# Kernel tuning notes

Measured on AMD Instinct MI355X. Metric: run time of the kernel, lower is better.

## Reference

```python
import jax, jax.numpy as jnp
import numpy as np

NUM_C = 100
DIM_S = 128
SIZE_M = 64
EMB = 128
MAX_CODE_LEN = 128
NODE_COUNT = 10000
PATH_COUNT = 10000
B, L = 16, 128


def setup_inputs() -> dict:
    key = jax.random.key(0)
    ks = jax.random.split(key, 24)
    def nrm(k, shape, fan):
        return jax.random.normal(k, shape, jnp.float32) * np.float32(np.sqrt(2.0 / fan))
    code = jax.random.randint(ks[0], (B, L, NUM_C * 2 + MAX_CODE_LEN * 3), 0, 10000)
    q = jax.random.randint(ks[1], (B, L), 0, NUM_C)
    r = jax.random.randint(ks[2], (B, L), 0, 2 * NUM_C)
    return {
        "code": code, "q": q, "r": r,
        "embed_nodes": nrm(ks[3], (NODE_COUNT + 2, EMB), EMB),
        "embed_paths": nrm(ks[4], (PATH_COUNT + 2, EMB), EMB),
        "W_pt": nrm(ks[5], (3 * EMB, 3 * EMB), 3 * EMB), "b_pt": jnp.zeros((3 * EMB,), jnp.float32),
        "W_att": nrm(ks[6], (3 * EMB, 1), 3 * EMB), "b_att": jnp.zeros((1,), jnp.float32),
        "k_emb": nrm(ks[7], (NUM_C + 1, DIM_S), DIM_S),
        "Mk": nrm(ks[8], (SIZE_M, DIM_S), DIM_S),
        "Mv0": nrm(ks[9], (SIZE_M, DIM_S), DIM_S),
        "v_emb": nrm(ks[10], (NUM_C * 2 + 2, DIM_S), DIM_S),
        "W_e": nrm(ks[11], (4 * DIM_S, DIM_S), 4 * DIM_S), "b_e": jnp.zeros((DIM_S,), jnp.float32),
        "W_a": nrm(ks[12], (4 * DIM_S, DIM_S), 4 * DIM_S), "b_a": jnp.zeros((DIM_S,), jnp.float32),
        "W_f": nrm(ks[13], (2 * DIM_S, DIM_S), 2 * DIM_S), "b_f": jnp.zeros((DIM_S,), jnp.float32),
        "W_p": nrm(ks[14], (DIM_S, 10), DIM_S), "b_p": jnp.zeros((10,), jnp.float32),
    }


def reference(code, q, r, embed_nodes, embed_paths, W_pt, b_pt, W_att, b_att,
              k_emb, Mk, Mv0, v_emb, W_e, b_e, W_a, b_a, W_f, b_f, W_p, b_p):
    bsz = code.shape[0]
    k = k_emb[q]                                    # [B,L,D]
    vr = v_emb[r]                                   # [B,L,D]
    # code2vec path triples: [B,L,MAX_CODE_LEN,3] = (start, path, end)
    c2v = code[:, :, NUM_C * 2:].reshape(bsz, code.shape[1], MAX_CODE_LEN, 3)
    full = jnp.concatenate([embed_nodes[c2v[..., 0]],
                            embed_nodes[c2v[..., 2]],
                            embed_paths[c2v[..., 1]]], axis=3)   # [B,L,P,3E]
    tr = jnp.tanh(full @ W_pt + b_pt)
    cw = tr @ W_att + b_att                          # [B,L,P,1]
    attn = jax.nn.softmax(cw, axis=1)                # faithful: softmax over seq dim (dim=1)
    code_vec = jnp.sum(full * attn, axis=2)          # [B,L,3E]
    v = jnp.concatenate([vr, code_vec], axis=2)      # [B,L,4D]
    w = jax.nn.softmax(k @ Mk.T, axis=-1)            # [B,L,M]
    e = jax.nn.sigmoid(v @ W_e + b_e)                # [B,L,D]
    a = jnp.tanh(v @ W_a + b_a)                      # [B,L,D]
    Mvt0 = jnp.broadcast_to(Mv0, (bsz,) + Mv0.shape) # [B,M,D]

    def step(Mvt, inp):
        et, at, wt = inp                             # [B,D],[B,D],[B,M]
        read = jnp.einsum('bm,bmd->bd', wt, Mvt)     # read pre-update memory (Mv[:, :-1])
        Mvt = Mvt * (1.0 - wt[:, :, None] * et[:, None, :]) + wt[:, :, None] * at[:, None, :]
        return Mvt, read

    _, reads = jax.lax.scan(step, Mvt0,
                            (e.transpose(1, 0, 2), a.transpose(1, 0, 2), w.transpose(1, 0, 2)))
    read = reads.transpose(1, 0, 2)                  # [B,L,D]
    f = jnp.tanh(jnp.concatenate([read, k], axis=-1) @ W_f + b_f)
    # dropout is identity in eval mode
    return jax.nn.sigmoid(f @ W_p + b_p)             # [B,L,10]
```

## Files before the change

### kernel.cpp

```cpp
#include <hip/hip_runtime.h>


typedef unsigned char u8;
typedef unsigned short u16;
typedef unsigned int u32;
typedef __attribute__((ext_vector_type(8))) short short8;
typedef __attribute__((ext_vector_type(4))) float f32x4;
typedef __attribute__((ext_vector_type(2))) float f32x2;

#define DEV __device__ __forceinline__
#define LOG2E 1.4426950408889634f

DEV u16 f2b(float f) {
    union { float f; u32 i; } v; v.f = f;
    u32 x = v.i;
    u32 r = (x + 0x7FFFu + ((x >> 16) & 1u)) >> 16;
    return (u16)r;
}
DEV float nexp(float x) { return __builtin_amdgcn_exp2f(x * LOG2E); }
DEV float nrcp(float x) { return __builtin_amdgcn_rcpf(x); }
DEV float fast_tanh(float x) {
    return 1.f - 2.f * nrcp(1.f + __builtin_amdgcn_exp2f(x * (2.f * LOG2E)));
}
DEV float sigmoidf_(float x) { return nrcp(1.f + __builtin_amdgcn_exp2f(-x * LOG2E)); }
DEV f32x2 d8(u32 x, bool hi) {
    return hi ? __builtin_amdgcn_cvt_pk_f32_fp8((int)x, true)
              : __builtin_amdgcn_cvt_pk_f32_fp8((int)x, false);
}
DEV u8 e8(float x) {
    return (u8)(__builtin_amdgcn_cvt_pk_fp8_f32(x, x, 0, false) & 0xFF);
}

__global__ void k_conv(const float* __restrict__ EN, const float* __restrict__ EP,
                       const float* __restrict__ Wpt, const float* __restrict__ We,
                       const float* __restrict__ Wa, const float* __restrict__ Wf,
                       const float* __restrict__ Wp,
                       u16* __restrict__ ENb, u16* __restrict__ EPb, u16* __restrict__ Wt,
                       u16* __restrict__ WeaT, u16* __restrict__ WfT, u16* __restrict__ WpT,
                       u8* __restrict__ EN8, u8* __restrict__ EP8) {
    const int NE = 10002 * 128;
    const int T0 = 2 * NE;
    const int T1 = T0 + 147456;
    const int T2 = T1 + 131072;
    const int T3 = T2 + 32768;
    const int T4 = T3 + 2048;
    const int T5 = T4 + NE / 2;
    const int T6 = T5 + NE / 2;
    for (int i = blockIdx.x * blockDim.x + threadIdx.x; i < T6; i += gridDim.x * blockDim.x) {
        if (i < NE) {
            ENb[i] = f2b(EN[i]);
        } else if (i < T0) {
            EPb[i - NE] = f2b(EP[i - NE]);
        } else if (i < T1) {
            int w = i - T0;  u32 n = (u32)w / 384u, k = (u32)w % 384u;
            Wt[w] = f2b(Wpt[k * 384 + n]);
        } else if (i < T2) {
            int w = i - T1;  int n = w >> 9, k = w & 511;
            WeaT[w] = f2b((n < 128) ? We[k * 128 + n] : Wa[k * 128 + (n - 128)]);
        } else if (i < T3) {
            int w = i - T2;  int n = w >> 8, k = w & 255;
            WfT[w] = f2b(Wf[k * 128 + n]);
        } else if (i < T4) {
            int w = i - T3;  int n = w >> 7, k = w & 127;
            WpT[w] = (n < 10) ? f2b(Wp[k * 10 + n]) : (u16)0;
        } else if (i < T5) {
            int j = i - T4;
            int pk = __builtin_amdgcn_cvt_pk_fp8_f32(EN[2 * j], EN[2 * j + 1], 0, false);
            ((u16*)EN8)[j] = (u16)pk;
        } else {
            int j = i - T5;
            int pk = __builtin_amdgcn_cvt_pk_fp8_f32(EP[2 * j], EP[2 * j + 1], 0, false);
            ((u16*)EP8)[j] = (u16)pk;
        }
    }
}

__global__ void k_wsm(const float* __restrict__ Kemb, const float* __restrict__ Mk,
                      float* __restrict__ wsmall) {
    int row = blockIdx.x;
    int m = threadIdx.x;
    __shared__ float kr[128];
    kr[m] = Kemb[row * 128 + m];
    kr[64 + m] = Kemb[row * 128 + 64 + m];
    __syncthreads();
    float lg = 0.f;
    for (int k = 0; k < 128; k += 8) {
        float mk8[8];
#pragma unroll
        for (int u = 0; u < 8; u++) mk8[u] = Mk[m * 128 + k + u];
#pragma unroll
        for (int u = 0; u < 8; u++) lg = fmaf(kr[k + u], mk8[u], lg);
    }
    float mx = lg;
#pragma unroll
    for (int off = 32; off; off >>= 1) mx = fmaxf(mx, __shfl_xor(mx, off, 64));
    float ex = nexp(lg - mx);
    float sum = ex;
#pragma unroll
    for (int off = 32; off; off >>= 1) sum += __shfl_xor(sum, off, 64);
    wsmall[row * 64 + m] = ex * nrcp(sum);
}

__global__ void k_preM(const u16* __restrict__ ENb, const u16* __restrict__ EPb,
                       const u16* __restrict__ Wt, const float* __restrict__ bpt,
                       u8* __restrict__ PS8, u8* __restrict__ PE8, u8* __restrict__ PP8) {
    int which = blockIdx.y;
    int r0 = blockIdx.x * 16;
    int wv = threadIdx.x >> 6, lane = threadIdx.x & 63;
    int m = lane & 15, quad = lane >> 4;
    const u16* A = (which == 2) ? EPb : ENb;
    int koff = which * 128;
    u8* dst = (which == 0) ? PS8 : (which == 1) ? PE8 : PP8;

    const short8* ap = (const short8*)(A + (r0 + m) * 128 + quad * 8);
    short8 a0 = ap[0], a1 = ap[4], a2 = ap[8], a3 = ap[12];

    for (int nt = 0; nt < 6; nt++) {
        int n0 = wv * 96 + nt * 16;
        const short8* bp = (const short8*)(Wt + (n0 + m) * 384 + koff + quad * 8);
        f32x4 acc = {0.f, 0.f, 0.f, 0.f};
        acc = __builtin_amdgcn_mfma_f32_16x16x32_bf16(a0, bp[0],  acc, 0, 0, 0);
        acc = __builtin_amdgcn_mfma_f32_16x16x32_bf16(a1, bp[4],  acc, 0, 0, 0);
        acc = __builtin_amdgcn_mfma_f32_16x16x32_bf16(a2, bp[8],  acc, 0, 0, 0);
        acc = __builtin_amdgcn_mfma_f32_16x16x32_bf16(a3, bp[12], acc, 0, 0, 0);
        int col = n0 + m;
        float bias = (which == 2) ? bpt[col] : 0.f;
#pragma unroll
        for (int reg = 0; reg < 4; reg++) {
            int row = r0 + quad * 4 + reg;
            if (row < 10002) dst[row * 384 + col] = e8(acc[reg] + bias);
        }
    }
}

__global__ void k_cw(const int* __restrict__ code,
                     const u8* __restrict__ PS8, const u8* __restrict__ PE8,
                     const u8* __restrict__ PP8, const float* __restrict__ Watt,
                     const float* __restrict__ batt, float* __restrict__ cw) {
    int wv = threadIdx.x >> 6, lane = threadIdx.x & 63;
    int t0 = (blockIdx.x * 4 + wv) * 4;
    int b = t0 >> 14;
    int rem = t0 & 16383;
    int l = rem >> 7, p0 = rem & 127;

    const int* c = code + ((b * 128 + l) * 584 + 200 + 3 * p0);
    int si[4], pi[4], ei[4];
#pragma unroll
    for (int i = 0; i < 4; i++) {
        si[i] = __builtin_amdgcn_readfirstlane(c[3 * i]);
        pi[i] = __builtin_amdgcn_readfirstlane(c[3 * i + 1]);
        ei[i] = __builtin_amdgcn_readfirstlane(c[3 * i + 2]);
    }

    int j0 = 6 * lane;
    int o32 = j0 + ((lane & 1) << 1);
    int o16 = j0 + ((~lane & 1) << 2);
    float wa0 = Watt[o32], wa1 = Watt[o32 + 1], wa2 = Watt[o32 + 2], wa3 = Watt[o32 + 3];
    float wb0 = Watt[o16], wb1 = Watt[o16 + 1];
    float batt0 = batt[0];

#pragma unroll
    for (int i = 0; i < 4; i++) {
        const u8* bs = PS8 + si[i] * 384;
        const u8* be = PE8 + ei[i] * 384;
        const u8* bq = PP8 + pi[i] * 384;
        u32 xs = *(const u32*)(bs + o32), ys = *(const u16*)(bs + o16);
        u32 xe = *(const u32*)(be + o32), ye = *(const u16*)(be + o16);
        u32 xq = *(const u32*)(bq + o32), yq = *(const u16*)(bq + o16);

        f32x2 zA = d8(xs, false) + d8(xe, false) + d8(xq, false);
        f32x2 zB = d8(xs, true)  + d8(xe, true)  + d8(xq, true);
        f32x2 zC = d8(ys, false) + d8(ye, false) + d8(yq, false);

        float acc = 0.f;
        acc = fmaf(fast_tanh(zA.x), wa0, acc);
        acc = fmaf(fast_tanh(zA.y), wa1, acc);
        acc = fmaf(fast_tanh(zB.x), wa2, acc);
        acc = fmaf(fast_tanh(zB.y), wa3, acc);
        acc = fmaf(fast_tanh(zC.x), wb0, acc);
        acc = fmaf(fast_tanh(zC.y), wb1, acc);

#pragma unroll
        for (int off = 32; off; off >>= 1) acc += __shfl_down(acc, off, 64);
        if (lane == 0) cw[(b * 128 + p0 + i) * 128 + l] = acc + batt0;
    }
}

__global__ void k_sm(const float* __restrict__ cw, float* __restrict__ attn) {
    int b = blockIdx.x >> 3, p0 = (blockIdx.x & 7) * 16;
    int tid = threadIdx.x;
    int wv = tid >> 6, lane = tid & 63;
    __shared__ float tile[16][128];
    __shared__ float atile[128][17];
    for (int idx = tid; idx < 2048; idx += 256) {
        int pp = idx >> 7, l = idx & 127;
        tile[pp][l] = cw[(b * 128 + p0 + pp) * 128 + l];
    }
    __syncthreads();
#pragma unroll
    for (int pl = 0; pl < 4; pl++) {
        int pp = wv * 4 + pl;
        float x0 = tile[pp][lane], x1 = tile[pp][64 + lane];
        float mx = fmaxf(x0, x1);
#pragma unroll
        for (int off = 32; off; off >>= 1) mx = fmaxf(mx, __shfl_xor(mx, off, 64));
        float e0 = nexp(x0 - mx), e1 = nexp(x1 - mx);
        float sum = e0 + e1;
#pragma unroll
        for (int off = 32; off; off >>= 1) sum += __shfl_xor(sum, off, 64);
        float inv = nrcp(sum);
        atile[lane][pp] = e0 * inv;
        atile[64 + lane][pp] = e1 * inv;
    }
    __syncthreads();
    for (int idx = tid; idx < 2048; idx += 256) {
        int l = idx >> 4, pp = idx & 15;
        attn[(b * 128 + l) * 128 + p0 + pp] = atile[l][pp];
    }
}

__global__ void k_cv(const int* __restrict__ code, const float* __restrict__ attn,
                     const u8* __restrict__ EN8, const u8* __restrict__ EP8,
                     const int* __restrict__ rr, const int* __restrict__ qq,
                     const float* __restrict__ Vemb, const float* __restrict__ Kemb,
                     u16* __restrict__ vA, u16* __restrict__ fA) {
    int row = blockIdx.x;
    int tid = threadIdx.x;
    int wv = tid >> 6, lane = tid & 63;
    __shared__ int si[128], ei[128], pi[128];
    __shared__ float at[128];
    __shared__ float part[4][3][128];
    if (tid < 128) {
        const int* c = code + (row * 584 + 200);
        si[tid] = c[3 * tid]; pi[tid] = c[3 * tid + 1]; ei[tid] = c[3 * tid + 2];
        at[tid] = attn[row * 128 + tid];
    }
    if (tid < 128) {
        vA[row * 512 + tid] = f2b(Vemb[rr[row] * 128 + tid]);
    } else {
        int t2 = tid - 128;
        fA[row * 256 + 128 + t2] = f2b(Kemb[qq[row] * 128 + t2]);
    }
    __syncthreads();
    float a0 = 0.f, a1 = 0.f, b0 = 0.f, b1 = 0.f, c0 = 0.f, c1 = 0.f;
    int o = 2 * lane;
    for (int p = wv; p < 128; p += 8) {
        int p2 = p + 4;
        float w = at[p], w2 = at[p2];
        u32 us = *(const u16*)(EN8 + si[p] * 128 + o);
        u32 ue = *(const u16*)(EN8 + ei[p] * 128 + o);
        u32 up = *(const u16*)(EP8 + pi[p] * 128 + o);
        u32 vs = *(const u16*)(EN8 + si[p2] * 128 + o);
        u32 ve = *(const u16*)(EN8 + ei[p2] * 128 + o);
        u32 vp = *(const u16*)(EP8 + pi[p2] * 128 + o);
        f32x2 fs = d8(us, false), fe = d8(ue, false), fp = d8(up, false);
        f32x2 gs = d8(vs, false), ge = d8(ve, false), gp = d8(vp, false);
        a0 = fmaf(w, fs.x, a0); a1 = fmaf(w, fs.y, a1);
        b0 = fmaf(w, fe.x, b0); b1 = fmaf(w, fe.y, b1);
        c0 = fmaf(w, fp.x, c0); c1 = fmaf(w, fp.y, c1);
        a0 = fmaf(w2, gs.x, a0); a1 = fmaf(w2, gs.y, a1);
        b0 = fmaf(w2, ge.x, b0); b1 = fmaf(w2, ge.y, b1);
        c0 = fmaf(w2, gp.x, c0); c1 = fmaf(w2, gp.y, c1);
    }
    part[wv][0][2 * lane] = a0; part[wv][0][2 * lane + 1] = a1;
    part[wv][1][2 * lane] = b0; part[wv][1][2 * lane + 1] = b1;
    part[wv][2][2 * lane] = c0; part[wv][2][2 * lane + 1] = c1;
    __syncthreads();
    u16* vrow = vA + row * 512 + 128;
    for (int idx = tid; idx < 384; idx += 256) {
        int tbl = idx >> 7, col = idx & 127;
        vrow[idx] = f2b(part[0][tbl][col] + part[1][tbl][col] + part[2][tbl][col] + part[3][tbl][col]);
    }
}

__global__ void k_eawM(const u16* __restrict__ vA, const u16* __restrict__ WeaT,
                       const float* __restrict__ be, const float* __restrict__ ba,
                       float* __restrict__ eb, float* __restrict__ ab) {
    int rt = blockIdx.x >> 2, cg = blockIdx.x & 3;
    int wv = threadIdx.x >> 6, lane = threadIdx.x & 63;
    int ct = cg * 4 + wv;
    int m = lane & 15, quad = lane >> 4;
    const short8* ap = (const short8*)(vA + (rt * 16 + m) * 512 + quad * 8);
    const short8* bp = (const short8*)(WeaT + (ct * 16 + m) * 512 + quad * 8);
    f32x4 acc = {0.f, 0.f, 0.f, 0.f};
#pragma unroll
    for (int kc = 0; kc < 16; kc++)
        acc = __builtin_amdgcn_mfma_f32_16x16x32_bf16(ap[kc * 4], bp[kc * 4], acc, 0, 0, 0);
    int col = ct * 16 + m;
    bool isA = col >= 128;
    int c2 = isA ? col - 128 : col;
    float bias = isA ? ba[c2] : be[c2];
#pragma unroll
    for (int reg = 0; reg < 4; reg++) {
        int row = rt * 16 + quad * 4 + reg;
        float val = acc[reg] + bias;
        if (isA) ab[row * 128 + c2] = fast_tanh(val);
        else     eb[row * 128 + c2] = sigmoidf_(val);
    }
}

__global__ void k_scan(const float* __restrict__ Mv0, const float* __restrict__ eb,
                       const float* __restrict__ ab, const float* __restrict__ wsmall,
                       const int* __restrict__ qq, u16* __restrict__ fA) {
    int b = blockIdx.x >> 4, dblk = blockIdx.x & 15;
    int lane = threadIdx.x;
    int s = lane >> 3, dlo = lane & 7;
    int d = dblk * 8 + dlo;

    __shared__ float wsm[101 * 64];
    __shared__ float el[128][8];
    __shared__ float al[128][8];
    __shared__ int ql[128];

    for (int i = lane; i < 101 * 64; i += 64) wsm[i] = wsmall[i];
    for (int i = lane; i < 1024; i += 64) {
        int t = i >> 3, dl = i & 7;
        el[t][dl] = eb[(b * 128 + t) * 128 + dblk * 8 + dl];
        al[t][dl] = ab[(b * 128 + t) * 128 + dblk * 8 + dl];
    }
    for (int i = lane; i < 128; i += 64) ql[i] = qq[b * 128 + i];
    __syncthreads();

    float mv[8];
#pragma unroll
    for (int q = 0; q < 8; q++) mv[q] = Mv0[(s * 8 + q) * 128 + d];

    u16* fout = fA + (b * 128) * 256 + d;

    int qt = ql[0];
    const float4* wr = (const float4*)(wsm + qt * 64 + s * 8);
    float4 w0 = wr[0], w1 = wr[1];
    float ecur = el[0][dlo], acur = al[0][dlo];

    for (int t = 0; t < 128; t++) {
        int tn = (t < 127) ? t + 1 : 127;
        int qn = ql[tn];
        const float4* wrn = (const float4*)(wsm + qn * 64 + s * 8);
        float4 nw0 = wrn[0], nw1 = wrn[1];
        float en = el[tn][dlo], an = al[tn][dlo];

        float w[8] = { w0.x, w0.y, w0.z, w0.w, w1.x, w1.y, w1.z, w1.w };
        float rd = 0.f;
#pragma unroll
        for (int q = 0; q < 8; q++) {
            rd = fmaf(w[q], mv[q], rd);
            mv[q] = fmaf(w[q], fmaf(-mv[q], ecur, acur), mv[q]);
        }
        rd += __shfl_xor(rd, 8, 64);
        rd += __shfl_xor(rd, 16, 64);
        rd += __shfl_xor(rd, 32, 64);
        if (s == 0) fout[t * 256] = f2b(rd);

        ecur = en; acur = an; w0 = nw0; w1 = nw1;
    }
}

__global__ void k_outM(const u16* __restrict__ fA, const u16* __restrict__ WfT,
                       const float* __restrict__ bfp, u16* __restrict__ gA) {
    int rt = blockIdx.x >> 1, cg = blockIdx.x & 1;
    int wv = threadIdx.x >> 6, lane = threadIdx.x & 63;
    int ct = cg * 4 + wv;
    int m = lane & 15, quad = lane >> 4;
    const short8* ap = (const short8*)(fA + (rt * 16 + m) * 256 + quad * 8);
    const short8* bp = (const short8*)(WfT + (ct * 16 + m) * 256 + quad * 8);
    f32x4 acc = {0.f, 0.f, 0.f, 0.f};
#pragma unroll
    for (int kc = 0; kc < 8; kc++)
        acc = __builtin_amdgcn_mfma_f32_16x16x32_bf16(ap[kc * 4], bp[kc * 4], acc, 0, 0, 0);
    int col = ct * 16 + m;
    float bias = bfp[col];
#pragma unroll
    for (int reg = 0; reg < 4; reg++) {
        int row = rt * 16 + quad * 4 + reg;
        gA[row * 128 + col] = f2b(fast_tanh(acc[reg] + bias));
    }
}

__global__ void k_fin(const u16* __restrict__ gA, const u16* __restrict__ WpT,
                      const float* __restrict__ bp, float* __restrict__ out) {
    int wv = threadIdx.x >> 6, lane = threadIdx.x & 63;
    int rt = blockIdx.x * 4 + wv;
    int m = lane & 15, quad = lane >> 4;
    const short8* ap = (const short8*)(gA + (rt * 16 + m) * 128 + quad * 8);
    const short8* bp8 = (const short8*)(WpT + m * 128 + quad * 8);
    f32x4 acc = {0.f, 0.f, 0.f, 0.f};
#pragma unroll
    for (int kc = 0; kc < 4; kc++)
        acc = __builtin_amdgcn_mfma_f32_16x16x32_bf16(ap[kc * 4], bp8[kc * 4], acc, 0, 0, 0);
    if (m < 10) {
        float bias = bp[m];
#pragma unroll
        for (int reg = 0; reg < 4; reg++) {
            int row = rt * 16 + quad * 4 + reg;
            out[row * 10 + m] = sigmoidf_(acc[reg] + bias);
        }
    }
}

extern "C" void kernel_launch(void* const* d_in, const int* in_sizes, int n_in,
                              void* d_out, int out_size, void* d_ws, size_t ws_size,
                              hipStream_t stream) {
    const int*   code = (const int*)d_in[0];
    const int*   q    = (const int*)d_in[1];
    const int*   r    = (const int*)d_in[2];
    const float* EN   = (const float*)d_in[3];
    const float* EP   = (const float*)d_in[4];
    const float* Wpt  = (const float*)d_in[5];
    const float* bpt  = (const float*)d_in[6];
    const float* Watt = (const float*)d_in[7];
    const float* batt = (const float*)d_in[8];
    const float* Kemb = (const float*)d_in[9];
    const float* Mk   = (const float*)d_in[10];
    const float* Mv0  = (const float*)d_in[11];
    const float* Vemb = (const float*)d_in[12];
    const float* We   = (const float*)d_in[13];
    const float* be   = (const float*)d_in[14];
    const float* Wa   = (const float*)d_in[15];
    const float* ba   = (const float*)d_in[16];
    const float* Wf   = (const float*)d_in[17];
    const float* bf_  = (const float*)d_in[18];
    const float* Wp   = (const float*)d_in[19];
    const float* bp   = (const float*)d_in[20];

    char* ws = (char*)d_ws;
    size_t off = 0;
    auto alloc = [&](size_t bytes) { void* p = ws + off; off = (off + bytes + 255) & ~255UL; return p; };
    u8*    PS8    = (u8*)alloc(10002UL * 384);
    u8*    PE8    = (u8*)alloc(10002UL * 384);
    u8*    PP8    = (u8*)alloc(10002UL * 384);
    u16*   ENb    = (u16*)alloc(10002UL * 128 * 2);
    u16*   EPb    = (u16*)alloc(10016UL * 128 * 2);
    u8*    EN8    = (u8*)alloc(10002UL * 128);
    u8*    EP8    = (u8*)alloc(10002UL * 128);
    u16*   Wt     = (u16*)alloc(384UL * 384 * 2);
    u16*   WeaT   = (u16*)alloc(256UL * 512 * 2);
    u16*   WfT    = (u16*)alloc(128UL * 256 * 2);
    u16*   WpT    = (u16*)alloc(16UL * 128 * 2);
    float* cw     = (float*)alloc(16UL * 128 * 128 * 4);
    float* attn   = (float*)alloc(16UL * 128 * 128 * 4);
    u16*   vA     = (u16*)alloc(2048UL * 512 * 2);
    u16*   fA     = (u16*)alloc(2048UL * 256 * 2);
    u16*   gA     = (u16*)alloc(2048UL * 128 * 2);
    float* eb     = (float*)alloc(2048UL * 128 * 4);
    float* ab     = (float*)alloc(2048UL * 128 * 4);
    float* wsmall = (float*)alloc(101UL * 64 * 4);

    k_conv<<<2048, 256, 0, stream>>>(EN, EP, Wpt, We, Wa, Wf, Wp, ENb, EPb, Wt, WeaT, WfT, WpT, EN8, EP8);
    k_wsm<<<101, 64, 0, stream>>>(Kemb, Mk, wsmall);
    k_preM<<<dim3(626, 3), 256, 0, stream>>>(ENb, EPb, Wt, bpt, PS8, PE8, PP8);
    k_cw<<<16384, 256, 0, stream>>>(code, PS8, PE8, PP8, Watt, batt, cw);
    k_sm<<<128, 256, 0, stream>>>(cw, attn);
    k_cv<<<2048, 256, 0, stream>>>(code, attn, EN8, EP8, r, q, Vemb, Kemb, vA, fA);
    k_eawM<<<512, 256, 0, stream>>>(vA, WeaT, be, ba, eb, ab);
    k_scan<<<256, 64, 0, stream>>>(Mv0, eb, ab, wsmall, q, fA);
    k_outM<<<256, 256, 0, stream>>>(fA, WfT, bf_, gA);
    k_fin<<<32, 256, 0, stream>>>(gA, WpT, bp, (float*)d_out);
}
```

Baseline: 260.1 us.

## Fuse small kernels, batch cw gathers, fold tanh scale and drop constant softmax bias

Folds the k_wsm softmax into extra blocks of k_conv and merges the bf16 and fp8 embedding conversions into one pass over the fp32 tables. k_outM and k_fin become a single kernel that keeps the intermediate tile in shared memory. k_cw now handles 8 paths per wave with all gathers issued before compute, and folds the tanh 2*log2e scale into the fp8 precompute. It also drops the attention bias and rewrites tanh-dot as sigmoid weighted by -2*W, relying on softmax shift invariance. The aim is fewer launches, fewer global round trips and more memory-level parallelism, at the cost of more registers in k_cw and a small fp8 precision shift from the pre-scaling.

```diff
diff --git a/kernel.cpp b/kernel.cpp
--- a/kernel.cpp
+++ b/kernel.cpp
@@ -10,6 +10,7 @@
 
 #define DEV __device__ __forceinline__
 #define LOG2E 1.4426950408889634f
+#define KSCALE 2.8853900817779268f
 
 DEV u16 f2b(float f) {
     union { float f; u32 i; } v; v.f = f;
@@ -35,22 +36,50 @@
                        const float* __restrict__ Wpt, const float* __restrict__ We,
                        const float* __restrict__ Wa, const float* __restrict__ Wf,
                        const float* __restrict__ Wp,
-                       u16* __restrict__ ENb, u16* __restrict__ EPb, u16* __restrict__ Wt,
-                       u16* __restrict__ WeaT, u16* __restrict__ WfT, u16* __restrict__ WpT,
-                       u8* __restrict__ EN8, u8* __restrict__ EP8) {
-    const int NE = 10002 * 128;
-    const int T0 = 2 * NE;
+                       const float* __restrict__ Kemb, const float* __restrict__ Mk,
+                       u16* __restrict__ ENb, u16* __restrict__ EPb,
+                       u8* __restrict__ EN8, u8* __restrict__ EP8,
+                       u16* __restrict__ Wt, u16* __restrict__ WeaT,
+                       u16* __restrict__ WfT, u16* __restrict__ WpT,
+                       float* __restrict__ wsmall) {
+    if (blockIdx.x >= 2048) {
+        int wv = threadIdx.x >> 6, lane = threadIdx.x & 63;
+        int row = (blockIdx.x - 2048) * 4 + wv;
+        if (row >= 101) return;
+        float lg = 0.f;
+        for (int k = 0; k < 128; k += 8) {
+            float mk8[8];
+#pragma unroll
+            for (int u = 0; u < 8; u++) mk8[u] = Mk[lane * 128 + k + u];
+#pragma unroll
+            for (int u = 0; u < 8; u++) lg = fmaf(Kemb[row * 128 + k + u], mk8[u], lg);
+        }
+        float mx = lg;
+#pragma unroll
+        for (int off = 32; off; off >>= 1) mx = fmaxf(mx, __shfl_xor(mx, off, 64));
+        float ex = nexp(lg - mx);
+        float sum = ex;
+#pragma unroll
+        for (int off = 32; off; off >>= 1) sum += __shfl_xor(sum, off, 64);
+        wsmall[row * 64 + lane] = ex * nrcp(sum);
+        return;
+    }
+    const int NEH = 10002 * 64;
+    const int T0 = 2 * NEH;
     const int T1 = T0 + 147456;
     const int T2 = T1 + 131072;
     const int T3 = T2 + 32768;
     const int T4 = T3 + 2048;
-    const int T5 = T4 + NE / 2;
-    const int T6 = T5 + NE / 2;
-    for (int i = blockIdx.x * blockDim.x + threadIdx.x; i < T6; i += gridDim.x * blockDim.x) {
-        if (i < NE) {
-            ENb[i] = f2b(EN[i]);
+    for (int i = blockIdx.x * blockDim.x + threadIdx.x; i < T4; i += 2048 * blockDim.x) {
+        if (i < NEH) {
+            float a = EN[2 * i], b = EN[2 * i + 1];
+            ((u32*)ENb)[i] = ((u32)f2b(b) << 16) | f2b(a);
+            ((u16*)EN8)[i] = (u16)__builtin_amdgcn_cvt_pk_fp8_f32(a, b, 0, false);
         } else if (i < T0) {
-            EPb[i - NE] = f2b(EP[i - NE]);
+            int j = i - NEH;
+            float a = EP[2 * j], b = EP[2 * j + 1];
+            ((u32*)EPb)[j] = ((u32)f2b(b) << 16) | f2b(a);
+            ((u16*)EP8)[j] = (u16)__builtin_amdgcn_cvt_pk_fp8_f32(a, b, 0, false);
         } else if (i < T1) {
             int w = i - T0;  u32 n = (u32)w / 384u, k = (u32)w % 384u;
             Wt[w] = f2b(Wpt[k * 384 + n]);
@@ -60,45 +89,11 @@
         } else if (i < T3) {
             int w = i - T2;  int n = w >> 8, k = w & 255;
             WfT[w] = f2b(Wf[k * 128 + n]);
-        } else if (i < T4) {
+        } else {
             int w = i - T3;  int n = w >> 7, k = w & 127;
             WpT[w] = (n < 10) ? f2b(Wp[k * 10 + n]) : (u16)0;
-        } else if (i < T5) {
-            int j = i - T4;
-            int pk = __builtin_amdgcn_cvt_pk_fp8_f32(EN[2 * j], EN[2 * j + 1], 0, false);
-            ((u16*)EN8)[j] = (u16)pk;
-        } else {
-            int j = i - T5;
-            int pk = __builtin_amdgcn_cvt_pk_fp8_f32(EP[2 * j], EP[2 * j + 1], 0, false);
-            ((u16*)EP8)[j] = (u16)pk;
-        }
-    }
-}
-
-__global__ void k_wsm(const float* __restrict__ Kemb, const float* __restrict__ Mk,
-                      float* __restrict__ wsmall) {
-    int row = blockIdx.x;
-    int m = threadIdx.x;
-    __shared__ float kr[128];
-    kr[m] = Kemb[row * 128 + m];
-    kr[64 + m] = Kemb[row * 128 + 64 + m];
-    __syncthreads();
-    float lg = 0.f;
-    for (int k = 0; k < 128; k += 8) {
-        float mk8[8];
-#pragma unroll
-        for (int u = 0; u < 8; u++) mk8[u] = Mk[m * 128 + k + u];
-#pragma unroll
-        for (int u = 0; u < 8; u++) lg = fmaf(kr[k + u], mk8[u], lg);
-    }
-    float mx = lg;
-#pragma unroll
-    for (int off = 32; off; off >>= 1) mx = fmaxf(mx, __shfl_xor(mx, off, 64));
-    float ex = nexp(lg - mx);
-    float sum = ex;
-#pragma unroll
-    for (int off = 32; off; off >>= 1) sum += __shfl_xor(sum, off, 64);
-    wsmall[row * 64 + m] = ex * nrcp(sum);
+        }
+    }
 }
 
 __global__ void k_preM(const u16* __restrict__ ENb, const u16* __restrict__ EPb,
@@ -128,7 +123,7 @@
 #pragma unroll
         for (int reg = 0; reg < 4; reg++) {
             int row = r0 + quad * 4 + reg;
-            if (row < 10002) dst[row * 384 + col] = e8(acc[reg] + bias);
+            if (row < 10002) dst[row * 384 + col] = e8((acc[reg] + bias) * KSCALE);
         }
     }
 }
@@ -136,17 +131,17 @@
 __global__ void k_cw(const int* __restrict__ code,
                      const u8* __restrict__ PS8, const u8* __restrict__ PE8,
                      const u8* __restrict__ PP8, const float* __restrict__ Watt,
-                     const float* __restrict__ batt, float* __restrict__ cw) {
+                     float* __restrict__ cw) {
     int wv = threadIdx.x >> 6, lane = threadIdx.x & 63;
-    int t0 = (blockIdx.x * 4 + wv) * 4;
+    int t0 = (blockIdx.x * 4 + wv) * 8;
     int b = t0 >> 14;
     int rem = t0 & 16383;
     int l = rem >> 7, p0 = rem & 127;
 
     const int* c = code + ((b * 128 + l) * 584 + 200 + 3 * p0);
-    int si[4], pi[4], ei[4];
-#pragma unroll
-    for (int i = 0; i < 4; i++) {
+    int si[8], pi[8], ei[8];
+#pragma unroll
+    for (int i = 0; i < 8; i++) {
         si[i] = __builtin_amdgcn_readfirstlane(c[3 * i]);
         pi[i] = __builtin_amdgcn_readfirstlane(c[3 * i + 1]);
         ei[i] = __builtin_amdgcn_readfirstlane(c[3 * i + 2]);
@@ -155,34 +150,37 @@
     int j0 = 6 * lane;
     int o32 = j0 + ((lane & 1) << 1);
     int o16 = j0 + ((~lane & 1) << 2);
-    float wa0 = Watt[o32], wa1 = Watt[o32 + 1], wa2 = Watt[o32 + 2], wa3 = Watt[o32 + 3];
-    float wb0 = Watt[o16], wb1 = Watt[o16 + 1];
-    float batt0 = batt[0];
-
-#pragma unroll
-    for (int i = 0; i < 4; i++) {
+    float wa0 = -2.f * Watt[o32],     wa1 = -2.f * Watt[o32 + 1];
+    float wa2 = -2.f * Watt[o32 + 2], wa3 = -2.f * Watt[o32 + 3];
+    float wb0 = -2.f * Watt[o16],     wb1 = -2.f * Watt[o16 + 1];
+
+    u32 xs[8], ys[8], xe[8], ye[8], xq[8], yq[8];
+#pragma unroll
+    for (int i = 0; i < 8; i++) {
         const u8* bs = PS8 + si[i] * 384;
         const u8* be = PE8 + ei[i] * 384;
         const u8* bq = PP8 + pi[i] * 384;
-        u32 xs = *(const u32*)(bs + o32), ys = *(const u16*)(bs + o16);
-        u32 xe = *(const u32*)(be + o32), ye = *(const u16*)(be + o16);
-        u32 xq = *(const u32*)(bq + o32), yq = *(const u16*)(bq + o16);
-
-        f32x2 zA = d8(xs, false) + d8(xe, false) + d8(xq, false);
-        f32x2 zB = d8(xs, true)  + d8(xe, true)  + d8(xq, true);
-        f32x2 zC = d8(ys, false) + d8(ye, false) + d8(yq, false);
-
-        float acc = 0.f;
-        acc = fmaf(fast_tanh(zA.x), wa0, acc);
-        acc = fmaf(fast_tanh(zA.y), wa1, acc);
-        acc = fmaf(fast_tanh(zB.x), wa2, acc);
-        acc = fmaf(fast_tanh(zB.y), wa3, acc);
-        acc = fmaf(fast_tanh(zC.x), wb0, acc);
-        acc = fmaf(fast_tanh(zC.y), wb1, acc);
+        xs[i] = *(const u32*)(bs + o32); ys[i] = *(const u16*)(bs + o16);
+        xe[i] = *(const u32*)(be + o32); ye[i] = *(const u16*)(be + o16);
+        xq[i] = *(const u32*)(bq + o32); yq[i] = *(const u16*)(bq + o16);
+    }
+
+#pragma unroll
+    for (int i = 0; i < 8; i++) {
+        f32x2 zA = d8(xs[i], false) + d8(xe[i], false) + d8(xq[i], false);
+        f32x2 zB = d8(xs[i], true)  + d8(xe[i], true)  + d8(xq[i], true);
+        f32x2 zC = d8(ys[i], false) + d8(ye[i], false) + d8(yq[i], false);
+
+        float acc = nrcp(1.f + __builtin_amdgcn_exp2f(zA.x)) * wa0;
+        acc = fmaf(nrcp(1.f + __builtin_amdgcn_exp2f(zA.y)), wa1, acc);
+        acc = fmaf(nrcp(1.f + __builtin_amdgcn_exp2f(zB.x)), wa2, acc);
+        acc = fmaf(nrcp(1.f + __builtin_amdgcn_exp2f(zB.y)), wa3, acc);
+        acc = fmaf(nrcp(1.f + __builtin_amdgcn_exp2f(zC.x)), wb0, acc);
+        acc = fmaf(nrcp(1.f + __builtin_amdgcn_exp2f(zC.y)), wb1, acc);
 
 #pragma unroll
         for (int off = 32; off; off >>= 1) acc += __shfl_down(acc, off, 64);
-        if (lane == 0) cw[(b * 128 + p0 + i) * 128 + l] = acc + batt0;
+        if (lane == 0) cw[(b * 128 + p0 + i) * 128 + l] = acc;
     }
 }
 
@@ -355,44 +353,42 @@
     }
 }
 
-__global__ void k_outM(const u16* __restrict__ fA, const u16* __restrict__ WfT,
-                       const float* __restrict__ bfp, u16* __restrict__ gA) {
-    int rt = blockIdx.x >> 1, cg = blockIdx.x & 1;
+__global__ void k_outfin(const u16* __restrict__ fA, const u16* __restrict__ WfT,
+                         const float* __restrict__ bfp, const u16* __restrict__ WpT,
+                         const float* __restrict__ bp, float* __restrict__ out) {
+    int rt = blockIdx.x;
     int wv = threadIdx.x >> 6, lane = threadIdx.x & 63;
-    int ct = cg * 4 + wv;
     int m = lane & 15, quad = lane >> 4;
+    __shared__ u16 ftile[16][128];
+
     const short8* ap = (const short8*)(fA + (rt * 16 + m) * 256 + quad * 8);
-    const short8* bp = (const short8*)(WfT + (ct * 16 + m) * 256 + quad * 8);
+    const short8* bpw = (const short8*)(WfT + (wv * 16 + m) * 256 + quad * 8);
     f32x4 acc = {0.f, 0.f, 0.f, 0.f};
 #pragma unroll
     for (int kc = 0; kc < 8; kc++)
-        acc = __builtin_amdgcn_mfma_f32_16x16x32_bf16(ap[kc * 4], bp[kc * 4], acc, 0, 0, 0);
-    int col = ct * 16 + m;
+        acc = __builtin_amdgcn_mfma_f32_16x16x32_bf16(ap[kc * 4], bpw[kc * 4], acc, 0, 0, 0);
+    int col = wv * 16 + m;
     float bias = bfp[col];
 #pragma unroll
-    for (int reg = 0; reg < 4; reg++) {
-        int row = rt * 16 + quad * 4 + reg;
-        gA[row * 128 + col] = f2b(fast_tanh(acc[reg] + bias));
-    }
-}
-
-__global__ void k_fin(const u16* __restrict__ gA, const u16* __restrict__ WpT,
-                      const float* __restrict__ bp, float* __restrict__ out) {
-    int wv = threadIdx.x >> 6, lane = threadIdx.x & 63;
-    int rt = blockIdx.x * 4 + wv;
-    int m = lane & 15, quad = lane >> 4;
-    const short8* ap = (const short8*)(gA + (rt * 16 + m) * 128 + quad * 8);
-    const short8* bp8 = (const short8*)(WpT + m * 128 + quad * 8);
-    f32x4 acc = {0.f, 0.f, 0.f, 0.f};
-#pragma unroll
-    for (int kc = 0; kc < 4; kc++)
-        acc = __builtin_amdgcn_mfma_f32_16x16x32_bf16(ap[kc * 4], bp8[kc * 4], acc, 0, 0, 0);
-    if (m < 10) {
-        float bias = bp[m];
-#pragma unroll
-        for (int reg = 0; reg < 4; reg++) {
-            int row = rt * 16 + quad * 4 + reg;
-            out[row * 10 + m] = sigmoidf_(acc[reg] + bias);
+    for (int reg = 0; reg < 4; reg++)
+        ftile[quad * 4 + reg][col] = f2b(fast_tanh(acc[reg] + bias));
+    __syncthreads();
+
+    if (wv == 0) {
+        f32x4 facc = {0.f, 0.f, 0.f, 0.f};
+#pragma unroll
+        for (int kc = 0; kc < 4; kc++) {
+            short8 af = *(const short8*)(&ftile[m][kc * 32 + quad * 8]);
+            short8 bf = *(const short8*)(WpT + m * 128 + kc * 32 + quad * 8);
+            facc = __builtin_amdgcn_mfma_f32_16x16x32_bf16(af, bf, facc, 0, 0, 0);
+        }
+        if (m < 10) {
+            float bias2 = bp[m];
+#pragma unroll
+            for (int reg = 0; reg < 4; reg++) {
+                int row = rt * 16 + quad * 4 + reg;
+                out[row * 10 + m] = sigmoidf_(facc[reg] + bias2);
+            }
         }
     }
 }
@@ -408,7 +404,6 @@
     const float* Wpt  = (const float*)d_in[5];
     const float* bpt  = (const float*)d_in[6];
     const float* Watt = (const float*)d_in[7];
-    const float* batt = (const float*)d_in[8];
     const float* Kemb = (const float*)d_in[9];
     const float* Mk   = (const float*)d_in[10];
     const float* Mv0  = (const float*)d_in[11];
@@ -440,19 +435,17 @@
     float* attn   = (float*)alloc(16UL * 128 * 128 * 4);
     u16*   vA     = (u16*)alloc(2048UL * 512 * 2);
     u16*   fA     = (u16*)alloc(2048UL * 256 * 2);
-    u16*   gA     = (u16*)alloc(2048UL * 128 * 2);
     float* eb     = (float*)alloc(2048UL * 128 * 4);
     float* ab     = (float*)alloc(2048UL * 128 * 4);
     float* wsmall = (float*)alloc(101UL * 64 * 4);
 
-    k_conv<<<2048, 256, 0, stream>>>(EN, EP, Wpt, We, Wa, Wf, Wp, ENb, EPb, Wt, WeaT, WfT, WpT, EN8, EP8);
-    k_wsm<<<101, 64, 0, stream>>>(Kemb, Mk, wsmall);
+    k_conv<<<2048 + 26, 256, 0, stream>>>(EN, EP, Wpt, We, Wa, Wf, Wp, Kemb, Mk,
+                                          ENb, EPb, EN8, EP8, Wt, WeaT, WfT, WpT, wsmall);
     k_preM<<<dim3(626, 3), 256, 0, stream>>>(ENb, EPb, Wt, bpt, PS8, PE8, PP8);
-    k_cw<<<16384, 256, 0, stream>>>(code, PS8, PE8, PP8, Watt, batt, cw);
+    k_cw<<<8192, 256, 0, stream>>>(code, PS8, PE8, PP8, Watt, cw);
     k_sm<<<128, 256, 0, stream>>>(cw, attn);
     k_cv<<<2048, 256, 0, stream>>>(code, attn, EN8, EP8, r, q, Vemb, Kemb, vA, fA);
     k_eawM<<<512, 256, 0, stream>>>(vA, WeaT, be, ba, eb, ab);
     k_scan<<<256, 64, 0, stream>>>(Mv0, eb, ab, wsmall, q, fA);
-    k_outM<<<256, 256, 0, stream>>>(fA, WfT, bf_, gA);
-    k_fin<<<32, 256, 0, stream>>>(gA, WpT, bp, (float*)d_out);
-}
+    k_outfin<<<128, 512, 0, stream>>>(fA, WfT, bf_, WpT, bp, (float*)d_out);
+}
```

Result: no change. 258.2 us (-0.7%).
